# Optimization experiments

Measured on AMD Instinct MI355X. Metric: run time of the kernel, lower is better.

## Reference

```python
import jax, jax.numpy as jnp
import numpy as np

B, T, CODE_NUM, MED_NUM = 256, 32, 4880, 1000
CODE_SIZE, H, OUT = 128, 128, 4880


def setup_inputs() -> dict:
    key = jax.random.key(0)
    ks = jax.random.split(key, 16)
    code_x = (jax.random.uniform(ks[0], (B, T, CODE_NUM)) < 0.05).astype(jnp.float32)
    medicine_codes = (jax.random.uniform(ks[1], (B, T, MED_NUM)) < 0.02).astype(jnp.float32)
    divided = (jax.random.uniform(ks[2], (B, T, CODE_NUM)) < 0.05).astype(jnp.float32)
    neighbors = (jax.random.uniform(ks[3], (B, T, CODE_NUM)) < 0.05).astype(jnp.float32)
    lens = jax.random.randint(ks[4], (B,), 1, T + 1)
    s = lambda fan: 1.0 / np.sqrt(fan)
    c_emb = jax.random.normal(ks[5], (CODE_NUM, CODE_SIZE)) * s(CODE_SIZE)
    m_emb = jax.random.normal(ks[6], (MED_NUM, CODE_SIZE)) * s(CODE_SIZE)
    W_c = jax.random.normal(ks[7], (CODE_SIZE, H)) * s(CODE_SIZE)
    W_m = jax.random.normal(ks[8], (CODE_SIZE, H)) * s(CODE_SIZE)
    Wa = jax.random.normal(ks[9], (3 * H, 32)) * s(3 * H)
    ba = jnp.zeros((32,), jnp.float32)
    va = jax.random.normal(ks[10], (32,)) * s(32)
    W_cls = jax.random.normal(ks[11], (3 * H, OUT)) * s(3 * H)
    b_cls = jnp.zeros((OUT,), jnp.float32)
    return dict(code_x=code_x, divided=divided, neighbors=neighbors, lens=lens,
                medicine_codes=medicine_codes, c_emb=c_emb, m_emb=m_emb,
                W_c=W_c, W_m=W_m, Wa=Wa, ba=ba, va=va, W_cls=W_cls, b_cls=b_cls)


def _forward(code_x, medicine_codes, lens, c_emb, m_emb, W_c, W_m, Wa, ba, va, W_cls, b_cls):
    # hypergraph_part: transform code/med embeddings, aggregate active codes per visit
    Hc = jnp.tanh(c_emb @ W_c)                      # [code_num, H]
    Hm = jnp.tanh(m_emb @ W_m)                      # [med_num, H]
    sum_c = jnp.einsum('btc,ch->bth', code_x, Hc)   # masked sum over active dx codes
    sum_m = jnp.einsum('btm,mh->bth', medicine_codes, Hm)
    h_c = sum_c / jnp.clip(code_x.sum(-1, keepdims=True), 1.0, None)
    h_m = sum_m / jnp.clip(medicine_codes.sum(-1, keepdims=True), 1.0, None)
    repre = jnp.concatenate([h_c, h_m, h_c * h_m], axis=-1)  # [B,T,3H]
    # DotProductAttention over visits, masked by lens
    scores = jnp.einsum('btk,k->bt', jnp.tanh(repre @ Wa + ba), va)
    mask = jnp.arange(T)[None, :] < lens[:, None]
    attn = jax.nn.softmax(jnp.where(mask, scores, -1e9), axis=-1)
    ctx = jnp.einsum('bt,btd->bd', attn, repre)     # [B,3H]
    # Classifier (dropout=identity in eval) + sigmoid
    return jax.nn.sigmoid(ctx @ W_cls + b_cls)      # [B,OUT]


def reference(code_x, divided, neighbors, lens, medicine_codes, c_emb, m_emb,
              W_c, W_m, Wa, ba, va, W_cls, b_cls):
    # divided/neighbors feed the transition branch whose output is unused
    # in the original forward's final prediction path.
    return _forward(code_x, medicine_codes, lens, c_emb, m_emb,
                    W_c, W_m, Wa, ba, va, W_cls, b_cls)
```

## Files before the change

kernel.cpp:

```cpp
#include <hip/hip_runtime.h>
#include <hip/hip_bf16.h>
#include <math.h>

#define Bsz 256
#define Tn 32
#define CODEN 4880
#define MEDN 1000
#define Hdim 128
#define OUTN 4880
#define BT (Bsz*Tn)
#define R3H 384
#define NC4 (CODEN/4)
#define NM4 (MEDN/4)

__device__ inline int mbcnt64(unsigned long long m) {
  return __builtin_amdgcn_mbcnt_hi((unsigned)(m >> 32),
         __builtin_amdgcn_mbcnt_lo((unsigned)m, 0));
}

__device__ inline unsigned f2bf(float f) {
  unsigned u = __float_as_uint(f);
  return (u + 0x7fffu + ((u >> 16) & 1u)) >> 16;
}

__global__ __launch_bounds__(128) void k_emb(
    const float* __restrict__ c_emb, const float* __restrict__ m_emb,
    const float* __restrict__ W_c, const float* __restrict__ W_m,
    unsigned* __restrict__ Hc2, unsigned* __restrict__ Hm2) {
  int row = blockIdx.x;
  const float* emb; const float* W; unsigned* out2;
  if (row < CODEN) { emb = c_emb + (size_t)row * Hdim; W = W_c; out2 = Hc2 + (size_t)row * 64; }
  else { int r = row - CODEN; emb = m_emb + (size_t)r * Hdim; W = W_m; out2 = Hm2 + (size_t)r * 64; }
  __shared__ float e[Hdim];
  int h = threadIdx.x;
  e[h] = emb[h];
  __syncthreads();
  float acc = 0.f;
#pragma unroll 8
  for (int k = 0; k < Hdim; ++k) acc += e[k] * W[k * Hdim + h];
  float vme = tanhf(acc);
  float vnx = __shfl_down(vme, 1, 64);
  if ((h & 1) == 0) out2[h >> 1] = f2bf(vme) | (f2bf(vnx) << 16);
}

#define MAXC 1024
#define MAXM 256

__global__ __launch_bounds__(256) void k_visit(
    const float* __restrict__ code_x, const float* __restrict__ med,
    const unsigned* __restrict__ Hc2, const unsigned* __restrict__ Hm2,
    const float* __restrict__ Wa, const float* __restrict__ ba,
    const float* __restrict__ va,
    float* __restrict__ repre, float* __restrict__ scores) {
  int bt = blockIdx.x;
  int tid = threadIdx.x;
  int lane = tid & 63;
  __shared__ int list_c[MAXC];
  __shared__ int list_m[MAXM];
  __shared__ int cnt_c, cnt_m;
  __shared__ float rep_s[R3H];
  __shared__ float red[512];
  if (tid == 0) { cnt_c = 0; cnt_m = 0; }
  __syncthreads();

  const float4* cx = (const float4*)(code_x + (size_t)bt * CODEN);
#pragma unroll
  for (int it = 0; it < 5; ++it) {
    int i = it * 256 + tid;
    float4 v = make_float4(0.f, 0.f, 0.f, 0.f);
    if (i < NC4) v = cx[i];
    unsigned long long m0 = __ballot(v.x != 0.f);
    unsigned long long m1 = __ballot(v.y != 0.f);
    unsigned long long m2 = __ballot(v.z != 0.f);
    unsigned long long m3 = __ballot(v.w != 0.f);
    int c0 = __popcll(m0), c1 = __popcll(m1), c2 = __popcll(m2), c3 = __popcll(m3);
    int base = 0;
    if (lane == 0) base = atomicAdd(&cnt_c, c0 + c1 + c2 + c3);
    base = __builtin_amdgcn_readfirstlane(base);
    int p;
    p = base + mbcnt64(m0);           if (v.x != 0.f && p < MAXC) list_c[p] = 4*i;
    p = base + c0 + mbcnt64(m1);      if (v.y != 0.f && p < MAXC) list_c[p] = 4*i+1;
    p = base + c0+c1 + mbcnt64(m2);   if (v.z != 0.f && p < MAXC) list_c[p] = 4*i+2;
    p = base + c0+c1+c2 + mbcnt64(m3);if (v.w != 0.f && p < MAXC) list_c[p] = 4*i+3;
  }
  {
    const float4* mx = (const float4*)(med + (size_t)bt * MEDN);
    int i = tid;
    float4 v = make_float4(0.f, 0.f, 0.f, 0.f);
    if (i < NM4) v = mx[i];
    unsigned long long m0 = __ballot(v.x != 0.f);
    unsigned long long m1 = __ballot(v.y != 0.f);
    unsigned long long m2 = __ballot(v.z != 0.f);
    unsigned long long m3 = __ballot(v.w != 0.f);
    int c0 = __popcll(m0), c1 = __popcll(m1), c2 = __popcll(m2), c3 = __popcll(m3);
    int base = 0;
    if (lane == 0) base = atomicAdd(&cnt_m, c0 + c1 + c2 + c3);
    base = __builtin_amdgcn_readfirstlane(base);
    int p;
    p = base + mbcnt64(m0);           if (v.x != 0.f && p < MAXM) list_m[p] = 4*i;
    p = base + c0 + mbcnt64(m1);      if (v.y != 0.f && p < MAXM) list_m[p] = 4*i+1;
    p = base + c0+c1 + mbcnt64(m2);   if (v.z != 0.f && p < MAXM) list_m[p] = 4*i+2;
    p = base + c0+c1+c2 + mbcnt64(m3);if (v.w != 0.f && p < MAXM) list_m[p] = 4*i+3;
  }
  __syncthreads();
  int nc = cnt_c < MAXC ? cnt_c : MAXC;
  int nm = cnt_m < MAXM ? cnt_m : MAXM;

  int g = tid >> 6, t = lane;
  float aCx = 0.f, aCy = 0.f;
#pragma unroll 4
  for (int j = g; j < nc; j += 4) {
    unsigned v = Hc2[(size_t)list_c[j] * 64 + t];
    aCx += __uint_as_float(v << 16);
    aCy += __uint_as_float(v & 0xffff0000u);
  }
  float aMx = 0.f, aMy = 0.f;
#pragma unroll 4
  for (int j = g; j < nm; j += 4) {
    unsigned v = Hm2[(size_t)list_m[j] * 64 + t];
    aMx += __uint_as_float(v << 16);
    aMy += __uint_as_float(v & 0xffff0000u);
  }

  red[g * 128 + 2 * t]     = aCx;
  red[g * 128 + 2 * t + 1] = aCy;
  __syncthreads();
  float hc = 0.f, hm = 0.f;
  if (tid < 128) {
    float s = red[tid] + red[128 + tid] + red[256 + tid] + red[384 + tid];
    hc = s / fmaxf((float)nc, 1.f);
  }
  __syncthreads();
  red[g * 128 + 2 * t]     = aMx;
  red[g * 128 + 2 * t + 1] = aMy;
  __syncthreads();
  if (tid < 128) {
    float s = red[tid] + red[128 + tid] + red[256 + tid] + red[384 + tid];
    hm = s / fmaxf((float)nm, 1.f);
    rep_s[tid]             = hc;
    rep_s[Hdim + tid]      = hm;
    rep_s[2 * Hdim + tid]  = hc * hm;
  }
  __syncthreads();

  float* rp = repre + (size_t)bt * R3H;
  for (int i = tid; i < R3H; i += 256) rp[i] = rep_s[i];

  int j = tid & 31, kc = tid >> 5;
  float pacc = 0.f;
  int k0 = kc * 48;
#pragma unroll 8
  for (int k = k0; k < k0 + 48; ++k) pacc += rep_s[k] * Wa[k * 32 + j];
  __syncthreads();
  red[tid] = pacc;
  __syncthreads();
  if (tid < 32) {
    float tot = 0.f;
#pragma unroll
    for (int c = 0; c < 8; ++c) tot += red[c * 32 + tid];
    float u = tanhf(tot + ba[tid]);
    float sv = u * va[tid];
#pragma unroll
    for (int off = 16; off >= 1; off >>= 1) sv += __shfl_down(sv, off, 32);
    if (tid == 0) scores[bt] = sv;
  }
}

__global__ __launch_bounds__(128) void k_ctx(
    const float* __restrict__ scores, const int* __restrict__ lens,
    const float* __restrict__ repre, float* __restrict__ ctx) {
  int b = blockIdx.x, tid = threadIdx.x;
  __shared__ float attn[Tn];
  int len = lens[b];
  if (tid < Tn) {
    float s = scores[b * Tn + tid];
    bool valid = tid < len;
    float sm = valid ? s : -1e30f;
    float m = sm;
#pragma unroll
    for (int off = 16; off >= 1; off >>= 1) m = fmaxf(m, __shfl_xor(m, off, 32));
    float e = valid ? expf(sm - m) : 0.f;
    float sum = e;
#pragma unroll
    for (int off = 16; off >= 1; off >>= 1) sum += __shfl_xor(sum, off, 32);
    attn[tid] = e / sum;
  }
  __syncthreads();
  const float* rp = repre + (size_t)b * Tn * R3H;
  for (int d = tid; d < R3H; d += 128) {
    float a = 0.f;
#pragma unroll
    for (int t = 0; t < Tn; ++t) a += attn[t] * rp[t * R3H + d];
    ctx[(size_t)b * R3H + d] = a;
  }
}

__device__ inline void fma4(float4& a, float s, const float4& w) {
  a.x += s * w.x; a.y += s * w.y; a.z += s * w.z; a.w += s * w.w;
}

__global__ __launch_bounds__(256) void k_cls(
    const float* __restrict__ ctx, const float* __restrict__ W_cls,
    const float* __restrict__ b_cls, float* __restrict__ out) {
  __shared__ float cs_t[R3H * 8];
  int tid = threadIdx.x;
  int ob = blockIdx.x % 5;
  int b0 = (blockIdx.x / 5) * 8;
  for (int i = tid; i < R3H * 8; i += 256) {
    int k = i >> 3, r = i & 7;
    cs_t[i] = ctx[(size_t)(b0 + r) * R3H + k];
  }
  __syncthreads();
  int o0 = ob * 1024 + tid * 4;
  if (o0 >= OUTN) return;
  float4 acc[8];
#pragma unroll
  for (int r = 0; r < 8; ++r) acc[r] = make_float4(0.f, 0.f, 0.f, 0.f);
  const float* wp = W_cls + o0;
  for (int k = 0; k < R3H; k += 8) {
    float4 wv[8];
#pragma unroll
    for (int u = 0; u < 8; ++u) wv[u] = *(const float4*)(wp + (size_t)(k + u) * OUTN);
#pragma unroll
    for (int u = 0; u < 8; ++u) {
      float4 cA = *(const float4*)&cs_t[(k + u) * 8];
      float4 cB = *(const float4*)&cs_t[(k + u) * 8 + 4];
      fma4(acc[0], cA.x, wv[u]); fma4(acc[1], cA.y, wv[u]);
      fma4(acc[2], cA.z, wv[u]); fma4(acc[3], cA.w, wv[u]);
      fma4(acc[4], cB.x, wv[u]); fma4(acc[5], cB.y, wv[u]);
      fma4(acc[6], cB.z, wv[u]); fma4(acc[7], cB.w, wv[u]);
    }
  }
  float4 bc = *(const float4*)(b_cls + o0);
#pragma unroll
  for (int r = 0; r < 8; ++r) {
    float4 v;
    v.x = 1.f / (1.f + expf(-(acc[r].x + bc.x)));
    v.y = 1.f / (1.f + expf(-(acc[r].y + bc.y)));
    v.z = 1.f / (1.f + expf(-(acc[r].z + bc.z)));
    v.w = 1.f / (1.f + expf(-(acc[r].w + bc.w)));
    *(float4*)(out + (size_t)(b0 + r) * OUTN + o0) = v;
  }
}

extern "C" void kernel_launch(void* const* d_in, const int* in_sizes, int n_in,
                              void* d_out, int out_size, void* d_ws, size_t ws_size,
                              hipStream_t stream) {
  const float* code_x = (const float*)d_in[0];
  const int*   lens   = (const int*)d_in[3];
  const float* med    = (const float*)d_in[4];
  const float* c_emb  = (const float*)d_in[5];
  const float* m_emb  = (const float*)d_in[6];
  const float* W_c    = (const float*)d_in[7];
  const float* W_m    = (const float*)d_in[8];
  const float* Wa     = (const float*)d_in[9];
  const float* ba     = (const float*)d_in[10];
  const float* va     = (const float*)d_in[11];
  const float* W_cls  = (const float*)d_in[12];
  const float* b_cls  = (const float*)d_in[13];
  float* out = (float*)d_out;
  float* ws  = (float*)d_ws;

  unsigned* Hc2    = (unsigned*)ws;
  unsigned* Hm2    = (unsigned*)ws + 312320;
  float*    repre  = ws + 376320;
  float*    scores = ws + 3522048;
  float*    ctx    = ws + 3530240;

  hipLaunchKernelGGL(k_emb,   dim3(CODEN + MEDN), dim3(128), 0, stream,
                     c_emb, m_emb, W_c, W_m, Hc2, Hm2);
  hipLaunchKernelGGL(k_visit, dim3(BT), dim3(256), 0, stream,
                     code_x, med, Hc2, Hm2, Wa, ba, va, repre, scores);
  hipLaunchKernelGGL(k_ctx,   dim3(Bsz), dim3(128), 0, stream,
                     scores, lens, repre, ctx);
  hipLaunchKernelGGL(k_cls,   dim3(160), dim3(256), 0, stream,
                     ctx, W_cls, b_cls, out);
}
```

Measured before the change: 535.8 us.

## Widen visit kernel to 512 threads with 8-byte gathers over 16 groups

Doubles the visit kernel's block size to 512 threads, so the code_x scan takes 3 iterations instead of 5. The embedding gather now uses 16 groups of 32 lanes, each loading 8 bytes (four bf16 values) with 32-bit byte offsets, accumulated into a float4 vector. The shared reduction buffer grows to hold 16 partials, and the attention projection is split over 16 chunks. The goal is more memory-level parallelism per visit for the dominant code_x read and the gathers, at the cost of more shared memory and possibly lower occupancy.

Result: no change. 533.1 us (-0.5%).

```diff
diff --git a/kernel.cpp b/kernel.cpp
--- a/kernel.cpp
+++ b/kernel.cpp
@@ -12,6 +12,8 @@
 #define R3H 384
 #define NC4 (CODEN/4)
 #define NM4 (MEDN/4)
+
+typedef __attribute__((ext_vector_type(4))) float f32x4;
 
 __device__ inline int mbcnt64(unsigned long long m) {
   return __builtin_amdgcn_mbcnt_hi((unsigned)(m >> 32),
@@ -46,7 +48,7 @@
 #define MAXC 1024
 #define MAXM 256
 
-__global__ __launch_bounds__(256) void k_visit(
+__global__ __launch_bounds__(512) void k_visit(
     const float* __restrict__ code_x, const float* __restrict__ med,
     const unsigned* __restrict__ Hc2, const unsigned* __restrict__ Hm2,
     const float* __restrict__ Wa, const float* __restrict__ ba,
@@ -59,105 +61,113 @@
   __shared__ int list_m[MAXM];
   __shared__ int cnt_c, cnt_m;
   __shared__ float rep_s[R3H];
-  __shared__ float red[512];
+  __shared__ float red[2048];
   if (tid == 0) { cnt_c = 0; cnt_m = 0; }
   __syncthreads();
 
-  const float4* cx = (const float4*)(code_x + (size_t)bt * CODEN);
-#pragma unroll
-  for (int it = 0; it < 5; ++it) {
-    int i = it * 256 + tid;
-    float4 v = make_float4(0.f, 0.f, 0.f, 0.f);
+  const uint4* cx = (const uint4*)(code_x + (size_t)bt * CODEN);
+#pragma unroll
+  for (int it = 0; it < 3; ++it) {
+    int i = it * 512 + tid;
+    uint4 v = make_uint4(0u, 0u, 0u, 0u);
     if (i < NC4) v = cx[i];
-    unsigned long long m0 = __ballot(v.x != 0.f);
-    unsigned long long m1 = __ballot(v.y != 0.f);
-    unsigned long long m2 = __ballot(v.z != 0.f);
-    unsigned long long m3 = __ballot(v.w != 0.f);
+    unsigned long long m0 = __ballot(v.x != 0u);
+    unsigned long long m1 = __ballot(v.y != 0u);
+    unsigned long long m2 = __ballot(v.z != 0u);
+    unsigned long long m3 = __ballot(v.w != 0u);
     int c0 = __popcll(m0), c1 = __popcll(m1), c2 = __popcll(m2), c3 = __popcll(m3);
     int base = 0;
     if (lane == 0) base = atomicAdd(&cnt_c, c0 + c1 + c2 + c3);
     base = __builtin_amdgcn_readfirstlane(base);
     int p;
-    p = base + mbcnt64(m0);           if (v.x != 0.f && p < MAXC) list_c[p] = 4*i;
-    p = base + c0 + mbcnt64(m1);      if (v.y != 0.f && p < MAXC) list_c[p] = 4*i+1;
-    p = base + c0+c1 + mbcnt64(m2);   if (v.z != 0.f && p < MAXC) list_c[p] = 4*i+2;
-    p = base + c0+c1+c2 + mbcnt64(m3);if (v.w != 0.f && p < MAXC) list_c[p] = 4*i+3;
+    p = base + mbcnt64(m0);            if (v.x != 0u && p < MAXC) list_c[p] = 4*i;
+    p = base + c0 + mbcnt64(m1);       if (v.y != 0u && p < MAXC) list_c[p] = 4*i+1;
+    p = base + c0+c1 + mbcnt64(m2);    if (v.z != 0u && p < MAXC) list_c[p] = 4*i+2;
+    p = base + c0+c1+c2 + mbcnt64(m3); if (v.w != 0u && p < MAXC) list_c[p] = 4*i+3;
   }
   {
-    const float4* mx = (const float4*)(med + (size_t)bt * MEDN);
+    const uint4* mx = (const uint4*)(med + (size_t)bt * MEDN);
     int i = tid;
-    float4 v = make_float4(0.f, 0.f, 0.f, 0.f);
+    uint4 v = make_uint4(0u, 0u, 0u, 0u);
     if (i < NM4) v = mx[i];
-    unsigned long long m0 = __ballot(v.x != 0.f);
-    unsigned long long m1 = __ballot(v.y != 0.f);
-    unsigned long long m2 = __ballot(v.z != 0.f);
-    unsigned long long m3 = __ballot(v.w != 0.f);
+    unsigned long long m0 = __ballot(v.x != 0u);
+    unsigned long long m1 = __ballot(v.y != 0u);
+    unsigned long long m2 = __ballot(v.z != 0u);
+    unsigned long long m3 = __ballot(v.w != 0u);
     int c0 = __popcll(m0), c1 = __popcll(m1), c2 = __popcll(m2), c3 = __popcll(m3);
     int base = 0;
     if (lane == 0) base = atomicAdd(&cnt_m, c0 + c1 + c2 + c3);
     base = __builtin_amdgcn_readfirstlane(base);
     int p;
-    p = base + mbcnt64(m0);           if (v.x != 0.f && p < MAXM) list_m[p] = 4*i;
-    p = base + c0 + mbcnt64(m1);      if (v.y != 0.f && p < MAXM) list_m[p] = 4*i+1;
-    p = base + c0+c1 + mbcnt64(m2);   if (v.z != 0.f && p < MAXM) list_m[p] = 4*i+2;
-    p = base + c0+c1+c2 + mbcnt64(m3);if (v.w != 0.f && p < MAXM) list_m[p] = 4*i+3;
+    p = base + mbcnt64(m0);            if (v.x != 0u && p < MAXM) list_m[p] = 4*i;
+    p = base + c0 + mbcnt64(m1);       if (v.y != 0u && p < MAXM) list_m[p] = 4*i+1;
+    p = base + c0+c1 + mbcnt64(m2);    if (v.z != 0u && p < MAXM) list_m[p] = 4*i+2;
+    p = base + c0+c1+c2 + mbcnt64(m3); if (v.w != 0u && p < MAXM) list_m[p] = 4*i+3;
   }
   __syncthreads();
   int nc = cnt_c < MAXC ? cnt_c : MAXC;
   int nm = cnt_m < MAXM ? cnt_m : MAXM;
 
-  int g = tid >> 6, t = lane;
-  float aCx = 0.f, aCy = 0.f;
+  int g = tid >> 5, t = tid & 31;
+  unsigned toff = (unsigned)t << 3;
+  const char* cb = (const char*)Hc2;
+  f32x4 aC = {0.f, 0.f, 0.f, 0.f};
 #pragma unroll 4
-  for (int j = g; j < nc; j += 4) {
-    unsigned v = Hc2[(size_t)list_c[j] * 64 + t];
-    aCx += __uint_as_float(v << 16);
-    aCy += __uint_as_float(v & 0xffff0000u);
-  }
-  float aMx = 0.f, aMy = 0.f;
-#pragma unroll 4
-  for (int j = g; j < nm; j += 4) {
-    unsigned v = Hm2[(size_t)list_m[j] * 64 + t];
-    aMx += __uint_as_float(v << 16);
-    aMy += __uint_as_float(v & 0xffff0000u);
-  }
-
-  red[g * 128 + 2 * t]     = aCx;
-  red[g * 128 + 2 * t + 1] = aCy;
+  for (int j = g; j < nc; j += 16) {
+    unsigned off = ((unsigned)list_c[j] << 8) + toff;
+    uint2 v = *(const uint2*)(cb + off);
+    f32x4 d = { __uint_as_float(v.x << 16), __uint_as_float(v.x & 0xffff0000u),
+                __uint_as_float(v.y << 16), __uint_as_float(v.y & 0xffff0000u) };
+    aC += d;
+  }
+  const char* mb = (const char*)Hm2;
+  f32x4 aM = {0.f, 0.f, 0.f, 0.f};
+  for (int j = g; j < nm; j += 16) {
+    unsigned off = ((unsigned)list_m[j] << 8) + toff;
+    uint2 v = *(const uint2*)(mb + off);
+    f32x4 d = { __uint_as_float(v.x << 16), __uint_as_float(v.x & 0xffff0000u),
+                __uint_as_float(v.y << 16), __uint_as_float(v.y & 0xffff0000u) };
+    aM += d;
+  }
+
+  ((f32x4*)red)[g * 32 + t] = aC;
   __syncthreads();
   float hc = 0.f, hm = 0.f;
   if (tid < 128) {
-    float s = red[tid] + red[128 + tid] + red[256 + tid] + red[384 + tid];
+    float s = 0.f;
+#pragma unroll
+    for (int gg = 0; gg < 16; ++gg) s += red[gg * 128 + tid];
     hc = s / fmaxf((float)nc, 1.f);
   }
   __syncthreads();
-  red[g * 128 + 2 * t]     = aMx;
-  red[g * 128 + 2 * t + 1] = aMy;
+  ((f32x4*)red)[g * 32 + t] = aM;
   __syncthreads();
   if (tid < 128) {
-    float s = red[tid] + red[128 + tid] + red[256 + tid] + red[384 + tid];
+    float s = 0.f;
+#pragma unroll
+    for (int gg = 0; gg < 16; ++gg) s += red[gg * 128 + tid];
     hm = s / fmaxf((float)nm, 1.f);
-    rep_s[tid]             = hc;
-    rep_s[Hdim + tid]      = hm;
-    rep_s[2 * Hdim + tid]  = hc * hm;
+    rep_s[tid]            = hc;
+    rep_s[Hdim + tid]     = hm;
+    rep_s[2 * Hdim + tid] = hc * hm;
   }
   __syncthreads();
 
   float* rp = repre + (size_t)bt * R3H;
-  for (int i = tid; i < R3H; i += 256) rp[i] = rep_s[i];
+  if (tid < R3H) rp[tid] = rep_s[tid];
 
   int j = tid & 31, kc = tid >> 5;
   float pacc = 0.f;
-  int k0 = kc * 48;
+  int k0 = kc * 24;
 #pragma unroll 8
-  for (int k = k0; k < k0 + 48; ++k) pacc += rep_s[k] * Wa[k * 32 + j];
+  for (int k = k0; k < k0 + 24; ++k) pacc += rep_s[k] * Wa[k * 32 + j];
   __syncthreads();
   red[tid] = pacc;
   __syncthreads();
   if (tid < 32) {
     float tot = 0.f;
 #pragma unroll
-    for (int c = 0; c < 8; ++c) tot += red[c * 32 + tid];
+    for (int c = 0; c < 16; ++c) tot += red[c * 32 + tid];
     float u = tanhf(tot + ba[tid]);
     float sv = u * va[tid];
 #pragma unroll
@@ -269,7 +279,7 @@
 
   hipLaunchKernelGGL(k_emb,   dim3(CODEN + MEDN), dim3(128), 0, stream,
                      c_emb, m_emb, W_c, W_m, Hc2, Hm2);
-  hipLaunchKernelGGL(k_visit, dim3(BT), dim3(256), 0, stream,
+  hipLaunchKernelGGL(k_visit, dim3(BT), dim3(512), 0, stream,
                      code_x, med, Hc2, Hm2, Wa, ba, va, repre, scores);
   hipLaunchKernelGGL(k_ctx,   dim3(Bsz), dim3(128), 0, stream,
                      scores, lens, repre, ctx);
```
